# Kernel tuning notes

Hardware: AMD Instinct MI355X
Metric: run time of the kernel (lower is better)

## Reference

```python
import jax, jax.numpy as jnp
import numpy as np

NUM_HEADS = 8
WINDOW = 64
ENCODERS = 6
EPS = 1e-5


def _positional_encoding(S, D, dtype=jnp.float32):
    pos = jnp.arange(S, dtype=jnp.float32)[:, None]
    div = jnp.exp(-jnp.log(10000.0) * jnp.arange(0, D, 2, dtype=jnp.float32) / D)
    ang = pos * div  # [S, D/2]
    pe = jnp.zeros((S, D), dtype=jnp.float32)
    pe = pe.at[:, 0::2].set(jnp.sin(ang)).at[:, 1::2].set(jnp.cos(ang))
    return pe.astype(dtype)


def _layernorm(x, g, b):
    mu = jnp.mean(x, axis=-1, keepdims=True)
    var = jnp.var(x, axis=-1, keepdims=True)
    return (x - mu) * jax.lax.rsqrt(var + EPS) * g + b


def _local_attention(x, wq, bq, wk, bk, wv, bv, window_mask):
    B, S, D = x.shape
    Dh = D // NUM_HEADS
    scale = Dh ** -0.5
    def split(t):  # [B,S,D] -> [B,H,S,Dh]
        return t.reshape(B, S, NUM_HEADS, Dh).transpose(0, 2, 1, 3)
    q = split(x @ wq.T + bq)
    k = split(x @ wk.T + bk)
    v = split(x @ wv.T + bv)
    scores = jnp.einsum('bhqd,bhkd->bhqk', q, k)
    # FAITHFUL: out-of-window entries are ZERO (not -inf); softmax over full S.
    scores = jnp.where(window_mask, scores, 0.0) * scale
    probs = jax.nn.softmax(scores, axis=-1)
    out = jnp.einsum('bhqk,bhkd->bhqd', probs, v)
    return out.transpose(0, 2, 1, 3).reshape(B, S, D)


def reference(inputs, emb, wq, bq, wk, bk, wv, bv, ln_g, ln_b,
              fc1_w, fc1_b, fc2_w, fc2_b, out_w, out_b):
    B, S = inputs.shape
    D = emb.shape[1]
    # window slice in torch source: [max(0, i-W), min(S, i+W))  (end exclusive)
    i = jnp.arange(S)[:, None]
    j = jnp.arange(S)[None, :]
    window_mask = (j >= i - WINDOW) & (j < i + WINDOW)  # [S, S]

    x = emb[inputs]  # [B, S, D]
    x = x + _positional_encoding(S, D, x.dtype)
    for _ in range(ENCODERS):  # shared weights across encoder iterations
        a = _local_attention(x, wq, bq, wk, bk, wv, bv, window_mask)
        x = _layernorm(a, ln_g, ln_b)
        h = jax.nn.relu(x @ fc1_w.T + fc1_b)
        x = (h @ fc2_w.T + fc2_b) + x
        x = _layernorm(x, ln_g, ln_b)
    x = x.reshape(B, S * D)
    return x @ out_w.T + out_b


def setup_inputs() -> dict:
    key = jax.random.key(0)
    ks = jax.random.split(key, 16)
    B, S, D, Hd, V, C = 8, 1024, 512, 2048, 32000, 6
    s = 0.02
    return {
        'inputs': jax.random.randint(ks[0], (B, S), 0, 31999),
        'emb': jax.random.normal(ks[1], (V, D), jnp.float32) * s,
        'wq': jax.random.normal(ks[2], (D, D), jnp.float32) * s,
        'bq': jnp.zeros((D,), jnp.float32),
        'wk': jax.random.normal(ks[3], (D, D), jnp.float32) * s,
        'bk': jnp.zeros((D,), jnp.float32),
        'wv': jax.random.normal(ks[4], (D, D), jnp.float32) * s,
        'bv': jnp.zeros((D,), jnp.float32),
        'ln_g': jnp.ones((D,), jnp.float32),
        'ln_b': jnp.zeros((D,), jnp.float32),
        'fc1_w': jax.random.normal(ks[5], (Hd, D), jnp.float32) * s,
        'fc1_b': jnp.zeros((Hd,), jnp.float32),
        'fc2_w': jax.random.normal(ks[6], (D, Hd), jnp.float32) * s,
        'fc2_b': jnp.zeros((D,), jnp.float32),
        'out_w': jax.random.normal(ks[7], (C, S * D), jnp.float32) * s,
        'out_b': jnp.zeros((C,), jnp.float32),
    }
```

## Files before the change

kernel.cpp:

```cpp
#include <hip/hip_runtime.h>

#define S_LEN 1024
#define DMODEL 512
#define NHEADS 8
#define DHEAD 64
#define HDIM 2048
#define WIN 64

typedef _Float16 f16x8 __attribute__((ext_vector_type(8)));
typedef _Float16 f16x2 __attribute__((ext_vector_type(2)));
typedef float f32x4 __attribute__((ext_vector_type(4)));
typedef float f32x16 __attribute__((ext_vector_type(16)));

__device__ __forceinline__ void stage16(const _Float16* g, _Float16* l) {
  __builtin_amdgcn_global_load_lds((const __attribute__((address_space(1))) unsigned int*)g,
                                   (__attribute__((address_space(3))) unsigned int*)l, 16, 0, 0);
}

__global__ void wprep_kernel(const float* __restrict__ wq, const float* __restrict__ wk,
                             const float* __restrict__ wv, const float* __restrict__ bq,
                             const float* __restrict__ bk, const float* __restrict__ bv,
                             const float* __restrict__ w1, const float* __restrict__ w2,
                             const float* __restrict__ wo,
                             _Float16* __restrict__ Wqkv, float* __restrict__ bqkv,
                             _Float16* __restrict__ W1h, _Float16* __restrict__ W2h,
                             _Float16* __restrict__ Woh) {
  int i = blockIdx.x * 256 + threadIdx.x;
  if (i < 262144) {
    Wqkv[i]          = (_Float16)wq[i];
    Wqkv[262144 + i] = (_Float16)wk[i];
    Wqkv[524288 + i] = (_Float16)wv[i];
  }
  if (i < 1048576) {
    W1h[i] = (_Float16)w1[i];
    W2h[i] = (_Float16)w2[i];
    Woh[i]           = (_Float16)wo[i];
    Woh[1048576 + i] = (_Float16)wo[1048576 + i];
    Woh[2097152 + i] = (_Float16)wo[2097152 + i];
  }
  if (i < 512) { bqkv[i] = bq[i]; bqkv[512 + i] = bk[i]; bqkv[1024 + i] = bv[i]; }
}

__global__ void embed_pe_kernel(const int* __restrict__ inputs, const float* __restrict__ emb,
                                _Float16* __restrict__ Xb, float* __restrict__ VS) {
  int row = blockIdx.x;
  int s = row & (S_LEN - 1);
  int t = threadIdx.x;
  if (row < 16) VS[row * 256 + t] = 0.0f;
  int tok = inputs[row];
  float dv = __expf(-logf(10000.0f) * (2.0f * (float)t) / (float)DMODEL);
  float ang = (float)s * dv;
  float sv = sinf(ang);
  float cv = cosf(ang);
  size_t base = (size_t)row * DMODEL + 2 * t;
  float x0 = emb[(size_t)tok * DMODEL + 2 * t] + sv;
  float x1 = emb[(size_t)tok * DMODEL + 2 * t + 1] + cv;
  f16x2 h; h[0] = (_Float16)x0; h[1] = (_Float16)x1;
  *(f16x2*)(Xb + base) = h;
}

#define EPI_RELU16 1
#define EPI_QKV 3
#define EPI_PART 4

template <int EPI>
__launch_bounds__(256)
__global__ void mfma_gemm(const _Float16* __restrict__ A, const _Float16* __restrict__ W,
                          const float* __restrict__ bias,
                          float* __restrict__ Pf0, float* __restrict__ Pf1,
                          _Float16* __restrict__ Ph2, _Float16* __restrict__ Ph3,
                          _Float16* __restrict__ Ch, float* __restrict__ VS,
                          int M, int N, int Kstride, int Kslice) {
  __shared__ _Float16 As[2][128 * 32];
  __shared__ _Float16 Bs[2][128 * 32];
  const int bm = blockIdx.x * 128;
  const int bn = blockIdx.y * 128;
  const int z = blockIdx.z;
  const int t = threadIdx.x;
  const int lane = t & 63;
  const int w = t >> 6;
  const int wr = w >> 1, wc = w & 1;
  const int l15 = lane & 15, l4 = lane >> 4;

  const int idx0 = t, idx1 = t + 256;
  const int r0 = idx0 >> 2, kg0 = (idx0 & 3) << 3;
  const int r1 = idx1 >> 2, kg1 = (idx1 & 3) << 3;
  const _Float16* Ag0 = A + (size_t)(bm + r0) * Kstride + kg0;
  const _Float16* Ag1 = A + (size_t)(bm + r1) * Kstride + kg1;
  const _Float16* Wg0 = W + (size_t)(bn + r0) * Kstride + kg0;
  const _Float16* Wg1 = W + (size_t)(bn + r1) * Kstride + kg1;

  const int kbeg = z * Kslice;
  const int nsteps = Kslice >> 5;

  stage16(Ag0 + kbeg, As[0] + idx0 * 8);
  stage16(Ag1 + kbeg, As[0] + idx1 * 8);
  stage16(Wg0 + kbeg, Bs[0] + idx0 * 8);
  stage16(Wg1 + kbeg, Bs[0] + idx1 * 8);
  __syncthreads();

  f32x4 acc[4][4] = {};
  int cur = 0;
  for (int s = 0; s < nsteps; ++s) {
    if (s + 1 < nsteps) {
      int kn = kbeg + (s + 1) * 32;
      stage16(Ag0 + kn, As[cur ^ 1] + idx0 * 8);
      stage16(Ag1 + kn, As[cur ^ 1] + idx1 * 8);
      stage16(Wg0 + kn, Bs[cur ^ 1] + idx0 * 8);
      stage16(Wg1 + kn, Bs[cur ^ 1] + idx1 * 8);
    }
    f16x8 af[4], bf[4];
#pragma unroll
    for (int m = 0; m < 4; ++m)
      af[m] = *(const f16x8*)&As[cur][(wr * 64 + m * 16 + l15) * 32 + l4 * 8];
#pragma unroll
    for (int n = 0; n < 4; ++n)
      bf[n] = *(const f16x8*)&Bs[cur][(wc * 64 + n * 16 + l15) * 32 + l4 * 8];
#pragma unroll
    for (int m = 0; m < 4; ++m)
#pragma unroll
      for (int n = 0; n < 4; ++n)
        acc[m][n] = __builtin_amdgcn_mfma_f32_16x16x32_f16(af[m], bf[n], acc[m][n], 0, 0, 0);
    __syncthreads();
    cur ^= 1;
  }

  float cs[4] = {0.f, 0.f, 0.f, 0.f};
#pragma unroll
  for (int n = 0; n < 4; ++n) {
    int col = bn + wc * 64 + n * 16 + l15;
    float bb = (EPI == EPI_PART) ? 0.f : bias[col];
#pragma unroll
    for (int m = 0; m < 4; ++m) {
      int row = bm + wr * 64 + m * 16 + l4 * 4;
#pragma unroll
      for (int j = 0; j < 4; ++j) {
        float v = acc[m][n][j] + bb;
        size_t off = (size_t)(row + j) * N + col;
        if (EPI == EPI_RELU16) {
          Ch[off] = (_Float16)fmaxf(v, 0.0f);
        } else if (EPI == EPI_QKV) {
          Ch[off] = (_Float16)v;
          cs[n] += v;
        } else {
          if (z == 0) Pf0[off] = v;
          else if (z == 1) Pf1[off] = v;
          else if (z == 2) Ph2[off] = (_Float16)v;
          else Ph3[off] = (_Float16)v;
        }
      }
    }
  }
  if (EPI == EPI_QKV && bn >= 1024) {
    const int batch = bm >> 10;
#pragma unroll
    for (int n = 0; n < 4; ++n) {
      float s = cs[n];
      s += __shfl_xor(s, 16);
      s += __shfl_xor(s, 32);
      if (l4 == 0) {
        int col = bn + wc * 64 + n * 16 + l15;
        atomicAdd(&VS[batch * 512 + (col - 1024)], s);
      }
    }
  }
}

#define KTMAX 256
#define VTS 264

__launch_bounds__(256)
__global__ void attn_kernel(const _Float16* __restrict__ QKVh, const float* __restrict__ VSg,
                            float* __restrict__ O) {
  __shared__ _Float16 Ks[KTMAX * 64];
  __shared__ _Float16 Vt[64 * VTS];
  __shared__ float VsC[8][64];

  const int qb0 = blockIdx.x * 128, h = blockIdx.y, b = blockIdx.z;
  const int jlo = max(0, qb0 - WIN);
  const int jhi = min(S_LEN, qb0 + 128 + WIN);
  const int KT = jhi - jlo;
  const int t = threadIdx.x;
  const int lane = t & 63, w = t >> 6;
  const int hi = lane >> 5, l31 = lane & 31;

  const _Float16* Kg = QKVh + ((size_t)(b * S_LEN + jlo)) * 1536 + 512 + h * 64;
#pragma unroll
  for (int p = 0; p < 8; ++p) {
    int u = t + p * 256;
    int row = u >> 3;
    int cb = (u & 7) * 16;
    int rowc = min(row, KT - 1);
    int scb = cb ^ ((row & 7) << 4);
    stage16(Kg + (size_t)rowc * 1536 + (scb >> 1), Ks + u * 8);
  }
  const _Float16* Vg = QKVh + ((size_t)(b * S_LEN + jlo)) * 1536 + 1024 + h * 64;
#pragma unroll
  for (int p = 0; p < 8; ++p) {
    int u = t + p * 256;
    int row = u >> 3;
    int d0 = (u & 7) * 8;
    f16x8 v = {0, 0, 0, 0, 0, 0, 0, 0};
    if (row < KT) v = *(const f16x8*)(Vg + (size_t)row * 1536 + d0);
#pragma unroll
    for (int e = 0; e < 8; ++e) Vt[(d0 + e) * VTS + row] = v[e];
  }
  __syncthreads();
  for (int slot = t; slot < 512; slot += 256) {
    int c = slot >> 6, d = slot & 63;
    const f16x8* col = (const f16x8*)(Vt + d * VTS + c * 32);
    float s = 0.f;
#pragma unroll
    for (int g = 0; g < 4; ++g) {
      f16x8 v = col[g];
#pragma unroll
      for (int e = 0; e < 8; ++e) s += (float)v[e];
    }
    VsC[c][d] = s;
  }
  const int qw = qb0 + w * 32;
  const _Float16* Qg = QKVh + ((size_t)(b * S_LEN + qw + l31)) * 1536 + h * 64;
  f16x8 qf[4];
#pragma unroll
  for (int ds = 0; ds < 4; ++ds) qf[ds] = *(const f16x8*)(Qg + ds * 16 + hi * 8);
  __syncthreads();

  const int c0 = max(0, qw - WIN - jlo) >> 5;
  const int c1 = min(KT, qw + 96 - jlo) >> 5;
  const int nproc = (c1 - c0) * 32;
  const int i = qw + l31;
  const int wlo = i - WIN, whi = i + WIN;

  float m = 0.f, l = 0.f;
  f32x16 accA = {}, accB = {};

  union PK { f16x2 h; unsigned u; };
  union A8 { unsigned u[4]; f16x8 h; };

  for (int c = c0; c < c1; ++c) {
    const int kb = c * 32;
    f32x16 sf = {};
#pragma unroll
    for (int ds = 0; ds < 4; ++ds) {
      int row = kb + l31;
      int cbyte = ((ds * 16 + hi * 8) * 2) ^ ((row & 7) << 4);
      f16x8 kf = *(const f16x8*)((const char*)Ks + row * 128 + cbyte);
      sf = __builtin_amdgcn_mfma_f32_32x32x16_f16(kf, qf[ds], sf, 0, 0, 0);
    }
    float s[16]; float pm = -1e30f;
#pragma unroll
    for (int r = 0; r < 16; ++r) {
      int gk = jlo + kb + (r & 3) + 8 * (r >> 2) + 4 * hi;
      float v = (gk >= wlo && gk < whi) ? sf[r] * 0.125f : 0.f;
      s[r] = v;
      pm = fmaxf(pm, v);
    }
    pm = fmaxf(pm, __shfl_xor(pm, 32));
    if (!__all(pm <= m + 8.f)) {
      float mn = fmaxf(m, pm);
      float f = __expf(m - mn);
      l *= f;
#pragma unroll
      for (int r = 0; r < 16; ++r) {
        int q = (r & 3) + 8 * (r >> 2) + 4 * hi;
        float fr = __shfl(f, q);
        accA[r] *= fr; accB[r] *= fr;
      }
      m = mn;
    }
    float p[16]; float ls = 0.f;
#pragma unroll
    for (int r = 0; r < 16; ++r) { p[r] = __expf(s[r] - m); ls += p[r]; }
    l += ls;
    unsigned u[8], x[8];
#pragma unroll
    for (int kk = 0; kk < 8; ++kk) {
      PK cv; cv.h[0] = (_Float16)p[2 * kk]; cv.h[1] = (_Float16)p[2 * kk + 1];
      u[kk] = cv.u;
    }
#pragma unroll
    for (int kk = 0; kk < 8; ++kk) x[kk] = (unsigned)__shfl_xor((int)u[kk], 32);
    A8 a0, a1;
    a0.u[0] = hi ? x[2] : u[0]; a0.u[1] = hi ? x[3] : u[1];
    a0.u[2] = hi ? u[2] : x[0]; a0.u[3] = hi ? u[3] : x[1];
    a1.u[0] = hi ? x[6] : u[4]; a1.u[1] = hi ? x[7] : u[5];
    a1.u[2] = hi ? u[6] : x[4]; a1.u[3] = hi ? u[7] : x[5];
#pragma unroll
    for (int ks = 0; ks < 2; ++ks) {
      f16x8 pa = ks ? a1.h : a0.h;
      f16x8 v0 = *(const f16x8*)(Vt + (size_t)(l31) * VTS + kb + ks * 16 + hi * 8);
      f16x8 v1 = *(const f16x8*)(Vt + (size_t)(32 + l31) * VTS + kb + ks * 16 + hi * 8);
      accA = __builtin_amdgcn_mfma_f32_32x32x16_f16(pa, v0, accA, 0, 0, 0);
      accB = __builtin_amdgcn_mfma_f32_32x32x16_f16(pa, v1, accB, 0, 0, 0);
    }
  }

  l = l + __shfl_xor(l, 32);
  const int dA = l31, dB = 32 + l31;
  float vsA = 0.f, vsB = 0.f;
  for (int c = c0; c < c1; ++c) { vsA += VsC[c][dA]; vsB += VsC[c][dB]; }
  const float vtA = VSg[b * 512 + h * 64 + dA];
  const float vtB = VSg[b * 512 + h * 64 + dB];
  const float zcount = (float)(S_LEN - nproc);
#pragma unroll
  for (int r = 0; r < 16; ++r) {
    int q = (r & 3) + 8 * (r >> 2) + 4 * hi;
    float mq = __shfl(m, q);
    float lq = __shfl(l, q);
    float em = __expf(-mq);
    float denom = lq + zcount * em;
    float inv = 1.0f / denom;
    size_t rowbase = ((size_t)(b * S_LEN + qw + q)) * DMODEL + h * 64;
    O[rowbase + dA] = (accA[r] + em * (vtA - vsA)) * inv;
    O[rowbase + dB] = (accB[r] + em * (vtB - vsB)) * inv;
  }
}

__global__ void ln_kernel(const float* __restrict__ X, const float* __restrict__ g,
                          const float* __restrict__ be, float* __restrict__ Y,
                          _Float16* __restrict__ Yh) {
  int row = blockIdx.x;
  int t = threadIdx.x;
  const float* x = X + (size_t)row * DMODEL;
  float2 v = *(const float2*)(x + 2 * t);
  float s = v.x + v.y;
  float sq = v.x * v.x + v.y * v.y;
#pragma unroll
  for (int off = 32; off; off >>= 1) {
    s += __shfl_xor(s, off);
    sq += __shfl_xor(sq, off);
  }
  __shared__ float ss[4], sqq[4];
  int w = t >> 6, lane = t & 63;
  if (lane == 0) { ss[w] = s; sqq[w] = sq; }
  __syncthreads();
  s = ss[0] + ss[1] + ss[2] + ss[3];
  sq = sqq[0] + sqq[1] + sqq[2] + sqq[3];
  float mu = s * (1.0f / DMODEL);
  float var = sq * (1.0f / DMODEL) - mu * mu;
  float rstd = rsqrtf(var + 1e-5f);
  float g0 = g[2 * t], g1 = g[2 * t + 1];
  float b0 = be[2 * t], b1 = be[2 * t + 1];
  float2 o;
  o.x = (v.x - mu) * rstd * g0 + b0;
  o.y = (v.y - mu) * rstd * g1 + b1;
  *(float2*)(Y + (size_t)row * DMODEL + 2 * t) = o;
  f16x2 hh; hh[0] = (_Float16)o.x; hh[1] = (_Float16)o.y;
  *(f16x2*)(Yh + (size_t)row * DMODEL + 2 * t) = hh;
}

__global__ void ln2_fused_kernel(const float* __restrict__ P0, const float* __restrict__ P1,
                                 const _Float16* __restrict__ P2h, const _Float16* __restrict__ P3h,
                                 const float* __restrict__ XB, const float* __restrict__ fb,
                                 const float* __restrict__ g, const float* __restrict__ be,
                                 _Float16* __restrict__ Yh, float* __restrict__ VS) {
  int row = blockIdx.x;
  int t = threadIdx.x;
  if (row < 16) VS[row * 256 + t] = 0.0f;
  size_t off = (size_t)row * DMODEL + 2 * t;
  float2 p0 = *(const float2*)(P0 + off);
  float2 p1 = *(const float2*)(P1 + off);
  f16x2 p2 = *(const f16x2*)(P2h + off);
  f16x2 p3 = *(const f16x2*)(P3h + off);
  float2 xb = *(const float2*)(XB + off);
  float2 v;
  v.x = p0.x + p1.x + (float)p2[0] + (float)p3[0] + fb[2 * t]     + xb.x;
  v.y = p0.y + p1.y + (float)p2[1] + (float)p3[1] + fb[2 * t + 1] + xb.y;
  float s = v.x + v.y;
  float sq = v.x * v.x + v.y * v.y;
#pragma unroll
  for (int off2 = 32; off2; off2 >>= 1) {
    s += __shfl_xor(s, off2);
    sq += __shfl_xor(sq, off2);
  }
  __shared__ float ss[4], sqq[4];
  int w = t >> 6, lane = t & 63;
  if (lane == 0) { ss[w] = s; sqq[w] = sq; }
  __syncthreads();
  s = ss[0] + ss[1] + ss[2] + ss[3];
  sq = sqq[0] + sqq[1] + sqq[2] + sqq[3];
  float mu = s * (1.0f / DMODEL);
  float var = sq * (1.0f / DMODEL) - mu * mu;
  float rstd = rsqrtf(var + 1e-5f);
  float g0 = g[2 * t], g1 = g[2 * t + 1];
  float b0 = be[2 * t], b1 = be[2 * t + 1];
  f16x2 hh;
  hh[0] = (_Float16)((v.x - mu) * rstd * g0 + b0);
  hh[1] = (_Float16)((v.y - mu) * rstd * g1 + b1);
  *(f16x2*)(Yh + off) = hh;
}

__global__ void outproj_partial_kernel(const _Float16* __restrict__ Xb,
                                       const _Float16* __restrict__ Woh,
                                       float* __restrict__ part) {
  const int KTOT = S_LEN * DMODEL;
  const int CH = KTOT / 32;
  int chunk = blockIdx.x, c = blockIdx.y, b = blockIdx.z;
  const int t = threadIdx.x;
  const _Float16* x = Xb + (size_t)b * KTOT + (size_t)chunk * CH;
  const _Float16* wv = Woh + (size_t)c * KTOT + (size_t)chunk * CH;
  float acc = 0.f;
#pragma unroll
  for (int p = 0; p < 8; ++p) {
    f16x8 a = *(const f16x8*)(x + (p * 256 + t) * 8);
    f16x8 w8 = *(const f16x8*)(wv + (p * 256 + t) * 8);
#pragma unroll
    for (int e = 0; e < 8; ++e) acc += (float)a[e] * (float)w8[e];
  }
#pragma unroll
  for (int off = 32; off; off >>= 1) acc += __shfl_xor(acc, off);
  __shared__ float red[4];
  int w = t >> 6, lane = t & 63;
  if (lane == 0) red[w] = acc;
  __syncthreads();
  if (t == 0)
    part[(b * 6 + c) * 32 + chunk] = red[0] + red[1] + red[2] + red[3];
}

__global__ void outproj_final_kernel(const float* __restrict__ part, const float* __restrict__ ob,
                                     float* __restrict__ out) {
  int idx = threadIdx.x;
  if (idx < 48) {
    float s = 0.f;
#pragma unroll
    for (int k = 0; k < 32; ++k) s += part[idx * 32 + k];
    out[idx] = s + ob[idx % 6];
  }
}

extern "C" void kernel_launch(void* const* d_in, const int* in_sizes, int n_in,
                              void* d_out, int out_size, void* d_ws, size_t ws_size,
                              hipStream_t stream) {
  (void)in_sizes; (void)n_in; (void)out_size; (void)ws_size;
  const int*   inputs = (const int*)  d_in[0];
  const float* emb    = (const float*)d_in[1];
  const float* wq     = (const float*)d_in[2];
  const float* bq     = (const float*)d_in[3];
  const float* wk     = (const float*)d_in[4];
  const float* bk     = (const float*)d_in[5];
  const float* wv     = (const float*)d_in[6];
  const float* bv     = (const float*)d_in[7];
  const float* ln_g   = (const float*)d_in[8];
  const float* ln_b   = (const float*)d_in[9];
  const float* fc1_w  = (const float*)d_in[10];
  const float* fc1_b  = (const float*)d_in[11];
  const float* fc2_w  = (const float*)d_in[12];
  const float* fc2_b  = (const float*)d_in[13];
  const float* out_w  = (const float*)d_in[14];
  const float* out_b  = (const float*)d_in[15];
  float* out = (float*)d_out;

  char* p = (char*)d_ws;
  float*    P0   = (float*)p;      p += (size_t)8192 * 512 * 4;
  _Float16* Xb   = (_Float16*)p;   p += (size_t)8192 * 512 * 2;
  _Float16* QKVh = (_Float16*)p;   p += (size_t)8192 * 1536 * 2;
  float*    XB   = (float*)p;      p += (size_t)8192 * 512 * 4;
  _Float16* XBb  = (_Float16*)p;   p += (size_t)8192 * 512 * 2;
  _Float16* H    = (_Float16*)p;   p += (size_t)8192 * 2048 * 2;
  float*    Ab   = (float*)H;
  _Float16* Wqkv = (_Float16*)p;   p += (size_t)1536 * 512 * 2;
  _Float16* W1h  = (_Float16*)p;   p += (size_t)2048 * 512 * 2;
  _Float16* W2h  = (_Float16*)p;   p += (size_t)512 * 2048 * 2;
  _Float16* Woh  = (_Float16*)p;   p += (size_t)6 * 524288 * 2;
  float*    bqkv = (float*)p;      p += 1536 * 4;
  float*    VS   = (float*)p;      p += 4096 * 4;
  float*    part = (float*)p;      p += 1536 * 4;
  float*    P1   = (float*)QKVh;
  _Float16* P2   = Xb;
  _Float16* P3   = XBb;

  wprep_kernel<<<4096, 256, 0, stream>>>(wq, wk, wv, bq, bk, bv, fc1_w, fc2_w, out_w,
                                         Wqkv, bqkv, W1h, W2h, Woh);
  embed_pe_kernel<<<8192, 256, 0, stream>>>(inputs, emb, Xb, VS);
  for (int it = 0; it < 6; ++it) {
    mfma_gemm<EPI_QKV><<<dim3(64, 12), 256, 0, stream>>>(Xb, Wqkv, bqkv,
        nullptr, nullptr, nullptr, nullptr, QKVh, VS, 8192, 1536, 512, 512);
    attn_kernel<<<dim3(8, 8, 8), 256, 0, stream>>>(QKVh, VS, Ab);
    ln_kernel<<<8192, 256, 0, stream>>>(Ab, ln_g, ln_b, XB, XBb);
    mfma_gemm<EPI_RELU16><<<dim3(64, 16), 256, 0, stream>>>(XBb, W1h, fc1_b,
        nullptr, nullptr, nullptr, nullptr, H, nullptr, 8192, 2048, 512, 512);
    mfma_gemm<EPI_PART><<<dim3(64, 4, 4), 256, 0, stream>>>(H, W2h, nullptr,
        P0, P1, P2, P3, nullptr, nullptr, 8192, 512, 2048, 512);
    ln2_fused_kernel<<<8192, 256, 0, stream>>>(P0, P1, P2, P3, XB, fc2_b,
                                               ln_g, ln_b, Xb, VS);
  }
  outproj_partial_kernel<<<dim3(32, 6, 8), 256, 0, stream>>>(Xb, Woh, part);
  outproj_final_kernel<<<1, 64, 0, stream>>>(part, out_b, out);
}
```

Baseline: 849.8 us.

## Store attention output and LN residual in fp16, use split-K of two for FC2

The attention output now goes out as fp16 instead of fp32, and the first layernorm keeps only the fp16 copy. The fp32 residual buffer XB is dropped, so the second layernorm reads the residual from XBb in fp16. The FC2 GEMM drops from four K-slices to two fp32 partials, which halves the partial-sum traffic but leaves fewer blocks to run in parallel. This cuts memory traffic across several kernels at the cost of precision in the residual path and less parallelism in FC2.

```diff
diff --git a/kernel.cpp b/kernel.cpp
--- a/kernel.cpp
+++ b/kernel.cpp
@@ -68,7 +68,6 @@
 __global__ void mfma_gemm(const _Float16* __restrict__ A, const _Float16* __restrict__ W,
                           const float* __restrict__ bias,
                           float* __restrict__ Pf0, float* __restrict__ Pf1,
-                          _Float16* __restrict__ Ph2, _Float16* __restrict__ Ph3,
                           _Float16* __restrict__ Ch, float* __restrict__ VS,
                           int M, int N, int Kstride, int Kslice) {
   __shared__ _Float16 As[2][128 * 32];
@@ -144,9 +143,7 @@
           cs[n] += v;
         } else {
           if (z == 0) Pf0[off] = v;
-          else if (z == 1) Pf1[off] = v;
-          else if (z == 2) Ph2[off] = (_Float16)v;
-          else Ph3[off] = (_Float16)v;
+          else Pf1[off] = v;
         }
       }
     }
@@ -171,7 +168,7 @@
 
 __launch_bounds__(256)
 __global__ void attn_kernel(const _Float16* __restrict__ QKVh, const float* __restrict__ VSg,
-                            float* __restrict__ O) {
+                            _Float16* __restrict__ O) {
   __shared__ _Float16 Ks[KTMAX * 64];
   __shared__ _Float16 Vt[64 * VTS];
   __shared__ float VsC[8][64];
@@ -311,20 +308,19 @@
     float denom = lq + zcount * em;
     float inv = 1.0f / denom;
     size_t rowbase = ((size_t)(b * S_LEN + qw + q)) * DMODEL + h * 64;
-    O[rowbase + dA] = (accA[r] + em * (vtA - vsA)) * inv;
-    O[rowbase + dB] = (accB[r] + em * (vtB - vsB)) * inv;
-  }
-}
-
-__global__ void ln_kernel(const float* __restrict__ X, const float* __restrict__ g,
-                          const float* __restrict__ be, float* __restrict__ Y,
-                          _Float16* __restrict__ Yh) {
+    O[rowbase + dA] = (_Float16)((accA[r] + em * (vtA - vsA)) * inv);
+    O[rowbase + dB] = (_Float16)((accB[r] + em * (vtB - vsB)) * inv);
+  }
+}
+
+__global__ void ln_kernel(const _Float16* __restrict__ X, const float* __restrict__ g,
+                          const float* __restrict__ be, _Float16* __restrict__ Yh) {
   int row = blockIdx.x;
   int t = threadIdx.x;
-  const float* x = X + (size_t)row * DMODEL;
-  float2 v = *(const float2*)(x + 2 * t);
-  float s = v.x + v.y;
-  float sq = v.x * v.x + v.y * v.y;
+  f16x2 v2 = *(const f16x2*)(X + (size_t)row * DMODEL + 2 * t);
+  float vx = (float)v2[0], vy = (float)v2[1];
+  float s = vx + vy;
+  float sq = vx * vx + vy * vy;
 #pragma unroll
   for (int off = 32; off; off >>= 1) {
     s += __shfl_xor(s, off);
@@ -341,17 +337,14 @@
   float rstd = rsqrtf(var + 1e-5f);
   float g0 = g[2 * t], g1 = g[2 * t + 1];
   float b0 = be[2 * t], b1 = be[2 * t + 1];
-  float2 o;
-  o.x = (v.x - mu) * rstd * g0 + b0;
-  o.y = (v.y - mu) * rstd * g1 + b1;
-  *(float2*)(Y + (size_t)row * DMODEL + 2 * t) = o;
-  f16x2 hh; hh[0] = (_Float16)o.x; hh[1] = (_Float16)o.y;
+  f16x2 hh;
+  hh[0] = (_Float16)((vx - mu) * rstd * g0 + b0);
+  hh[1] = (_Float16)((vy - mu) * rstd * g1 + b1);
   *(f16x2*)(Yh + (size_t)row * DMODEL + 2 * t) = hh;
 }
 
 __global__ void ln2_fused_kernel(const float* __restrict__ P0, const float* __restrict__ P1,
-                                 const _Float16* __restrict__ P2h, const _Float16* __restrict__ P3h,
-                                 const float* __restrict__ XB, const float* __restrict__ fb,
+                                 const _Float16* __restrict__ XBb, const float* __restrict__ fb,
                                  const float* __restrict__ g, const float* __restrict__ be,
                                  _Float16* __restrict__ Yh, float* __restrict__ VS) {
   int row = blockIdx.x;
@@ -360,14 +353,11 @@
   size_t off = (size_t)row * DMODEL + 2 * t;
   float2 p0 = *(const float2*)(P0 + off);
   float2 p1 = *(const float2*)(P1 + off);
-  f16x2 p2 = *(const f16x2*)(P2h + off);
-  f16x2 p3 = *(const f16x2*)(P3h + off);
-  float2 xb = *(const float2*)(XB + off);
-  float2 v;
-  v.x = p0.x + p1.x + (float)p2[0] + (float)p3[0] + fb[2 * t]     + xb.x;
-  v.y = p0.y + p1.y + (float)p2[1] + (float)p3[1] + fb[2 * t + 1] + xb.y;
-  float s = v.x + v.y;
-  float sq = v.x * v.x + v.y * v.y;
+  f16x2 xb = *(const f16x2*)(XBb + off);
+  float vx = p0.x + p1.x + fb[2 * t]     + (float)xb[0];
+  float vy = p0.y + p1.y + fb[2 * t + 1] + (float)xb[1];
+  float s = vx + vy;
+  float sq = vx * vx + vy * vy;
 #pragma unroll
   for (int off2 = 32; off2; off2 >>= 1) {
     s += __shfl_xor(s, off2);
@@ -385,8 +375,8 @@
   float g0 = g[2 * t], g1 = g[2 * t + 1];
   float b0 = be[2 * t], b1 = be[2 * t + 1];
   f16x2 hh;
-  hh[0] = (_Float16)((v.x - mu) * rstd * g0 + b0);
-  hh[1] = (_Float16)((v.y - mu) * rstd * g1 + b1);
+  hh[0] = (_Float16)((vx - mu) * rstd * g0 + b0);
+  hh[1] = (_Float16)((vy - mu) * rstd * g1 + b1);
   *(f16x2*)(Yh + off) = hh;
 }
 
@@ -454,10 +444,9 @@
   float*    P0   = (float*)p;      p += (size_t)8192 * 512 * 4;
   _Float16* Xb   = (_Float16*)p;   p += (size_t)8192 * 512 * 2;
   _Float16* QKVh = (_Float16*)p;   p += (size_t)8192 * 1536 * 2;
-  float*    XB   = (float*)p;      p += (size_t)8192 * 512 * 4;
   _Float16* XBb  = (_Float16*)p;   p += (size_t)8192 * 512 * 2;
   _Float16* H    = (_Float16*)p;   p += (size_t)8192 * 2048 * 2;
-  float*    Ab   = (float*)H;
+  _Float16* Abh  = H;
   _Float16* Wqkv = (_Float16*)p;   p += (size_t)1536 * 512 * 2;
   _Float16* W1h  = (_Float16*)p;   p += (size_t)2048 * 512 * 2;
   _Float16* W2h  = (_Float16*)p;   p += (size_t)512 * 2048 * 2;
@@ -466,22 +455,20 @@
   float*    VS   = (float*)p;      p += 4096 * 4;
   float*    part = (float*)p;      p += 1536 * 4;
   float*    P1   = (float*)QKVh;
-  _Float16* P2   = Xb;
-  _Float16* P3   = XBb;
 
   wprep_kernel<<<4096, 256, 0, stream>>>(wq, wk, wv, bq, bk, bv, fc1_w, fc2_w, out_w,
                                          Wqkv, bqkv, W1h, W2h, Woh);
   embed_pe_kernel<<<8192, 256, 0, stream>>>(inputs, emb, Xb, VS);
   for (int it = 0; it < 6; ++it) {
     mfma_gemm<EPI_QKV><<<dim3(64, 12), 256, 0, stream>>>(Xb, Wqkv, bqkv,
-        nullptr, nullptr, nullptr, nullptr, QKVh, VS, 8192, 1536, 512, 512);
-    attn_kernel<<<dim3(8, 8, 8), 256, 0, stream>>>(QKVh, VS, Ab);
-    ln_kernel<<<8192, 256, 0, stream>>>(Ab, ln_g, ln_b, XB, XBb);
+        nullptr, nullptr, QKVh, VS, 8192, 1536, 512, 512);
+    attn_kernel<<<dim3(8, 8, 8), 256, 0, stream>>>(QKVh, VS, Abh);
+    ln_kernel<<<8192, 256, 0, stream>>>(Abh, ln_g, ln_b, XBb);
     mfma_gemm<EPI_RELU16><<<dim3(64, 16), 256, 0, stream>>>(XBb, W1h, fc1_b,
-        nullptr, nullptr, nullptr, nullptr, H, nullptr, 8192, 2048, 512, 512);
-    mfma_gemm<EPI_PART><<<dim3(64, 4, 4), 256, 0, stream>>>(H, W2h, nullptr,
-        P0, P1, P2, P3, nullptr, nullptr, 8192, 512, 2048, 512);
-    ln2_fused_kernel<<<8192, 256, 0, stream>>>(P0, P1, P2, P3, XB, fc2_b,
+        nullptr, nullptr, H, nullptr, 8192, 2048, 512, 512);
+    mfma_gemm<EPI_PART><<<dim3(64, 4, 2), 256, 0, stream>>>(H, W2h, nullptr,
+        P0, P1, nullptr, nullptr, 8192, 512, 2048, 1024);
+    ln2_fused_kernel<<<8192, 256, 0, stream>>>(P0, P1, XBb, fc2_b,
                                                ln_g, ln_b, Xb, VS);
   }
   outproj_partial_kernel<<<dim3(32, 6, 8), 256, 0, stream>>>(Xb, Woh, part);
```

After: 751.4 us (median of 2 runs). 1.13x faster.
